# Kernel tuning notes

Measured on AMD Instinct MI355X. Metric: run time of the kernel, lower is better.

The kernel has to match this reference:

```python
import jax, jax.numpy as jnp
import numpy as np

N = 100000        # num nodes
E = 3200000       # num edges (avg degree 32)
C = 64            # num classes


def setup_inputs() -> dict:
    key = jax.random.key(0)
    k1, k2, k3 = jax.random.split(key, 3)
    edge_index = jax.random.randint(k1, (2, E), 0, N, dtype=jnp.int64)
    # Linear(N, C): weight [C, N]; we store its transpose Wt [N, C] for gather
    Wt = jax.random.normal(k2, (N, C), dtype=jnp.float32) * (1.0 / np.sqrt(N))
    b = jnp.zeros((C,), dtype=jnp.float32)
    return {"edge_index": edge_index, "Wt": Wt, "b": b}


def reference(edge_index, Wt, b):
    # logits[i] = sum_{(i,j) in edges} Wt[j] + b  == (A @ W.T + b)
    row, col = edge_index[0], edge_index[1]
    gathered = Wt[col]                                      # [E, C]
    logits = jax.ops.segment_sum(gathered, row, num_segments=N) + b  # [N, C]
    return jax.nn.log_softmax(logits, axis=1)
```

## Files before the change

kernel.cpp:

```cpp
#include <hip/hip_runtime.h>
#include <hip/hip_bf16.h>


#define C64 64
#define BROWS 64
#define LROW_SHIFT 17
#define COL_MASK 0x1FFFF
#define MAXNB 2048
#define SCAT_TPB 1024
#define SCAT_EPT2 8
#define SCAT_EDGES (SCAT_TPB * SCAT_EPT2 * 2)
#define CAPB 2432
#define GAT_TPB 512
#define FP8_SCALE 256.0f
#define FP8_ISCALE (1.0f / 256.0f)

typedef float v2f __attribute__((ext_vector_type(2)));

static __device__ __forceinline__ unsigned short f2bf(float f) {
    unsigned u = __float_as_uint(f);
    unsigned r = u + 0x7fff + ((u >> 16) & 1);
    return (unsigned short)(r >> 16);
}

__global__ __launch_bounds__(256) void LINK_cvt_bf16(const float* __restrict__ Wt,
                                                     unsigned short* __restrict__ Wtb,
                                                     int n4) {
    int i = blockIdx.x * blockDim.x + threadIdx.x;
    if (i >= n4) return;
    float4 v = ((const float4*)Wt)[i];
    ushort4 o;
    o.x = f2bf(v.x); o.y = f2bf(v.y); o.z = f2bf(v.z); o.w = f2bf(v.w);
    ((ushort4*)Wtb)[i] = o;
}

__global__ __launch_bounds__(SCAT_TPB) void LINK_cvt_scatter2(const float* __restrict__ Wt,
                                                              unsigned int* __restrict__ Wtq,
                                                              int n_u,
                                                              const int* __restrict__ ei,
                                                              int* __restrict__ cursor,
                                                              int* __restrict__ pk,
                                                              int E_, int nb, int nScat) {
    __shared__ int staged[SCAT_EDGES];
    __shared__ int h[MAXNB];
    __shared__ int lbase[MAXNB];
    __shared__ int loff[MAXNB + 1];
    __shared__ int part[SCAT_TPB];
    const int tid = threadIdx.x;

    if (blockIdx.x >= nScat) {
        int i = (blockIdx.x - nScat) * SCAT_TPB + tid;
        if (i < n_u) {
            float4 v = ((const float4*)Wt)[i];
            int p = __builtin_amdgcn_cvt_pk_fp8_f32(v.x * FP8_SCALE, v.y * FP8_SCALE, 0, false);
            p = __builtin_amdgcn_cvt_pk_fp8_f32(v.z * FP8_SCALE, v.w * FP8_SCALE, p, true);
            Wtq[i] = (unsigned)p;
        }
        return;
    }

    const int2* ei2r = (const int2*)ei;
    const int2* ei2c = (const int2*)(ei + E_);
    int2 rows[SCAT_EPT2];
    for (int i = tid; i < nb; i += SCAT_TPB) h[i] = 0;
    __syncthreads();
    const int base2 = blockIdx.x * (SCAT_TPB * SCAT_EPT2);
    const int E2 = E_ >> 1;
    #pragma unroll
    for (int i = 0; i < SCAT_EPT2; ++i) {
        int e2 = base2 + i * SCAT_TPB + tid;
        if (e2 < E2) {
            rows[i] = ei2r[e2];
            atomicAdd(&h[rows[i].x >> 6], 1);
            atomicAdd(&h[rows[i].y >> 6], 1);
        } else rows[i] = make_int2(-1, -1);
    }
    __syncthreads();

    const int chunk = (nb + SCAT_TPB - 1) / SCAT_TPB;
    const int cbeg = min(tid * chunk, nb);
    const int cend = min(cbeg + chunk, nb);
    int s = 0;
    for (int i = cbeg; i < cend; ++i) s += h[i];
    part[tid] = s;
    __syncthreads();
    for (int off = 1; off < SCAT_TPB; off <<= 1) {
        int v = (tid >= off) ? part[tid - off] : 0;
        __syncthreads();
        part[tid] += v;
        __syncthreads();
    }
    int run = (tid == 0) ? 0 : part[tid - 1];
    for (int i = cbeg; i < cend; ++i) {
        loff[i] = run;
        run += h[i];
    }
    if (tid == SCAT_TPB - 1) loff[nb] = run;
    __syncthreads();

    for (int i = tid; i < nb; i += SCAT_TPB) {
        int c = h[i];
        lbase[i] = c ? atomicAdd(&cursor[i], c) : 0;
        h[i] = 0;
    }
    __syncthreads();

    #pragma unroll
    for (int i = 0; i < SCAT_EPT2; ++i) {
        if (rows[i].x >= 0) {
            int e2 = base2 + i * SCAT_TPB + tid;
            int2 cols = ei2c[e2];
            int bkx = rows[i].x >> 6;
            int px = loff[bkx] + atomicAdd(&h[bkx], 1);
            staged[px] = ((rows[i].x & 63) << LROW_SHIFT) | cols.x;
            int bky = rows[i].y >> 6;
            int py = loff[bky] + atomicAdd(&h[bky], 1);
            staged[py] = ((rows[i].y & 63) << LROW_SHIFT) | cols.y;
        }
    }
    __syncthreads();

    const int cnt = loff[nb];
    for (int i = tid; i < cnt; i += SCAT_TPB) {
        int lo = 0, hi = nb;
        while (hi - lo > 1) {
            int mid = (lo + hi) >> 1;
            if (loff[mid] <= i) lo = mid; else hi = mid;
        }
        int gp = lbase[lo] + (i - loff[lo]);
        if (gp < CAPB) pk[lo * CAPB + gp] = staged[i];
    }
}

__global__ __launch_bounds__(SCAT_TPB) void LINK_scatter_big(const int* __restrict__ ei,
                                                             int* __restrict__ cursor,
                                                             int* __restrict__ pk,
                                                             int E_, int nb) {
    __shared__ int h[MAXNB];
    __shared__ int lbase[MAXNB];
    const int tid = threadIdx.x;
    const int2* ei2r = (const int2*)ei;
    const int2* ei2c = (const int2*)(ei + E_);
    int2 rows[SCAT_EPT2];
    for (int i = tid; i < nb; i += SCAT_TPB) h[i] = 0;
    __syncthreads();
    const int base2 = blockIdx.x * (SCAT_TPB * SCAT_EPT2);
    const int E2 = E_ >> 1;
    #pragma unroll
    for (int i = 0; i < SCAT_EPT2; ++i) {
        int e2 = base2 + i * SCAT_TPB + tid;
        if (e2 < E2) {
            rows[i] = ei2r[e2];
            atomicAdd(&h[rows[i].x >> 6], 1);
            atomicAdd(&h[rows[i].y >> 6], 1);
        } else rows[i] = make_int2(-1, -1);
    }
    __syncthreads();
    for (int i = tid; i < nb; i += SCAT_TPB) {
        int c = h[i];
        lbase[i] = c ? atomicAdd(&cursor[i], c) : 0;
    }
    __syncthreads();
    for (int i = tid; i < nb; i += SCAT_TPB) h[i] = 0;
    __syncthreads();
    #pragma unroll
    for (int i = 0; i < SCAT_EPT2; ++i) {
        if (rows[i].x >= 0) {
            int e2 = base2 + i * SCAT_TPB + tid;
            int2 cols = ei2c[e2];
            int bkx = rows[i].x >> 6;
            int lpx = lbase[bkx] + atomicAdd(&h[bkx], 1);
            if (lpx < CAPB) pk[bkx * CAPB + lpx] = ((rows[i].x & 63) << LROW_SHIFT) | cols.x;
            int bky = rows[i].y >> 6;
            int lpy = lbase[bky] + atomicAdd(&h[bky], 1);
            if (lpy < CAPB) pk[bky * CAPB + lpy] = ((rows[i].y & 63) << LROW_SHIFT) | cols.y;
        }
    }
}

__global__ __launch_bounds__(GAT_TPB) void LINK_binGather_f8(const int* __restrict__ cursor,
                                                             const int* __restrict__ pk,
                                                             const unsigned int* __restrict__ Wtq,
                                                             const float* __restrict__ b,
                                                             float* __restrict__ out,
                                                             int N_) {
    __shared__ int binned[CAPB];
    __shared__ int rcnt[BROWS];
    __shared__ int roff[BROWS];
    __shared__ int rcur[BROWS];
    const int tid = threadIdx.x;
    const int lane = tid & 63;
    const int li = lane & 15;
    const int quad = lane >> 4;
    const int w = tid >> 6;
    const int bkt = blockIdx.x;
    const int beg = bkt * CAPB;
    const int cnt = min(cursor[bkt], CAPB);

    if (tid < BROWS) rcnt[tid] = 0;
    __syncthreads();
    for (int i = tid; i < cnt; i += GAT_TPB) atomicAdd(&rcnt[pk[beg + i] >> LROW_SHIFT], 1);
    __syncthreads();
    if (tid < BROWS) {
        int v = rcnt[tid];
        int inc = v;
        #pragma unroll
        for (int d = 1; d < 64; d <<= 1) {
            int o = __shfl_up(inc, d);
            if (lane >= d) inc += o;
        }
        roff[tid] = inc - v;
        rcur[tid] = inc - v;
    }
    __syncthreads();
    for (int i = tid; i < cnt; i += GAT_TPB) {
        int p = pk[beg + i];
        int pos = atomicAdd(&rcur[p >> LROW_SHIFT], 1);
        binned[pos] = p & COL_MASK;
    }
    __syncthreads();

    const float4 bias = ((const float4*)b)[li];
    for (int r = w; r < BROWS; r += 8) {
        const int row = bkt * BROWS + r;
        if (row >= N_) break;
        const int off = roff[r];
        const int dg = rcnt[r];
        const int nq = dg >> 2;

        float a0 = 0.f, a1 = 0.f, a2 = 0.f, a3 = 0.f;
        int t = 0;
        for (; t + 8 <= nq; t += 8) {
            int cc[8];
            #pragma unroll
            for (int q = 0; q < 8; ++q) cc[q] = binned[off + 4 * (t + q) + quad];
            unsigned uu[8];
            #pragma unroll
            for (int q = 0; q < 8; ++q) uu[q] = Wtq[cc[q] * 16 + li];
            #pragma unroll
            for (int q = 0; q < 8; ++q) {
                v2f lo = __builtin_amdgcn_cvt_pk_f32_fp8((int)uu[q], false);
                v2f hi = __builtin_amdgcn_cvt_pk_f32_fp8((int)uu[q], true);
                a0 += lo[0]; a1 += lo[1]; a2 += hi[0]; a3 += hi[1];
            }
        }
        for (; t < nq; ++t) {
            int c = binned[off + 4 * t + quad];
            unsigned u = Wtq[c * 16 + li];
            v2f lo = __builtin_amdgcn_cvt_pk_f32_fp8((int)u, false);
            v2f hi = __builtin_amdgcn_cvt_pk_f32_fp8((int)u, true);
            a0 += lo[0]; a1 += lo[1]; a2 += hi[0]; a3 += hi[1];
        }
        const int rem = dg & 3;
        if (quad < rem) {
            int c = binned[off + 4 * nq + quad];
            unsigned u = Wtq[c * 16 + li];
            v2f lo = __builtin_amdgcn_cvt_pk_f32_fp8((int)u, false);
            v2f hi = __builtin_amdgcn_cvt_pk_f32_fp8((int)u, true);
            a0 += lo[0]; a1 += lo[1]; a2 += hi[0]; a3 += hi[1];
        }

        a0 += __shfl_xor(a0, 16); a0 += __shfl_xor(a0, 32);
        a1 += __shfl_xor(a1, 16); a1 += __shfl_xor(a1, 32);
        a2 += __shfl_xor(a2, 16); a2 += __shfl_xor(a2, 32);
        a3 += __shfl_xor(a3, 16); a3 += __shfl_xor(a3, 32);

        float x0 = a0 * FP8_ISCALE + bias.x;
        float x1 = a1 * FP8_ISCALE + bias.y;
        float x2 = a2 * FP8_ISCALE + bias.z;
        float x3 = a3 * FP8_ISCALE + bias.w;

        float m = fmaxf(fmaxf(x0, x1), fmaxf(x2, x3));
        #pragma unroll
        for (int mk = 1; mk < 16; mk <<= 1) m = fmaxf(m, __shfl_xor(m, mk));
        float s = __expf(x0 - m) + __expf(x1 - m) + __expf(x2 - m) + __expf(x3 - m);
        #pragma unroll
        for (int mk = 1; mk < 16; mk <<= 1) s += __shfl_xor(s, mk);
        float ls = logf(s);
        if (quad == 0) {
            float4 o;
            o.x = x0 - m - ls; o.y = x1 - m - ls; o.z = x2 - m - ls; o.w = x3 - m - ls;
            ((float4*)out)[row * 16 + li] = o;
        }
    }
}

__global__ __launch_bounds__(GAT_TPB) void LINK_binner(const int* __restrict__ cursor,
                                                       int* __restrict__ pk,
                                                       unsigned int* __restrict__ meta,
                                                       int N_) {
    __shared__ int stage[CAPB];
    __shared__ int binned[CAPB];
    __shared__ int rcnt[BROWS];
    __shared__ int roff[BROWS];
    __shared__ int rcur[BROWS];
    const int tid = threadIdx.x;
    const int lane = tid & 63;
    const int bkt = blockIdx.x;
    const int beg = bkt * CAPB;
    const int cnt = min(cursor[bkt], CAPB);

    if (tid < BROWS) rcnt[tid] = 0;
    for (int i = tid; i < cnt; i += GAT_TPB) stage[i] = pk[beg + i];
    __syncthreads();
    for (int i = tid; i < cnt; i += GAT_TPB) atomicAdd(&rcnt[stage[i] >> LROW_SHIFT], 1);
    __syncthreads();
    if (tid < BROWS) {
        int v = rcnt[tid];
        int inc = v;
        #pragma unroll
        for (int d = 1; d < 64; d <<= 1) {
            int o = __shfl_up(inc, d);
            if (lane >= d) inc += o;
        }
        roff[tid] = inc - v;
        rcur[tid] = inc - v;
    }
    __syncthreads();
    for (int i = tid; i < cnt; i += GAT_TPB) {
        int p = stage[i];
        int pos = atomicAdd(&rcur[p >> LROW_SHIFT], 1);
        binned[pos] = p & COL_MASK;
    }
    __syncthreads();
    for (int i = tid; i < cnt; i += GAT_TPB) pk[beg + i] = binned[i];
    if (tid < BROWS) {
        int row = bkt * BROWS + tid;
        if (row < N_)
            meta[row] = ((unsigned)(beg + roff[tid]) << 10) | (unsigned)min(rcnt[tid], 1023);
    }
}

__global__ __launch_bounds__(256) void LINK_gather_rows(const unsigned int* __restrict__ meta,
                                                        const int* __restrict__ scol,
                                                        const unsigned int* __restrict__ Wtu,
                                                        const float* __restrict__ b,
                                                        float* __restrict__ out,
                                                        int N_) {
    const int wid = (blockIdx.x * 256 + threadIdx.x) >> 6;
    const int nw = (gridDim.x * 256) >> 6;
    const int lane = threadIdx.x & 63;
    const int li = lane & 31;
    const int hi = lane >> 5;
    const float2 bias = ((const float2*)b)[li];

    for (int row = wid; row < N_; row += nw) {
        unsigned mt = meta[row];
        int beg = (int)(mt >> 10);
        int dg = (int)(mt & 1023);
        float l0 = 0.f, l1 = 0.f, l2 = 0.f, l3 = 0.f;
        float h0 = 0.f, h1 = 0.f, h2 = 0.f, h3 = 0.f;
        int npair = dg >> 1;
        int t = 0;
        for (; t + 8 <= npair; t += 8) {
            int cc[8];
            #pragma unroll
            for (int q = 0; q < 8; ++q) cc[q] = scol[beg + 2 * (t + q) + hi];
            unsigned uu[8];
            #pragma unroll
            for (int q = 0; q < 8; ++q) uu[q] = Wtu[cc[q] * 32 + li];
            l0 += __uint_as_float(uu[0] << 16); h0 += __uint_as_float(uu[0] & 0xffff0000u);
            l1 += __uint_as_float(uu[1] << 16); h1 += __uint_as_float(uu[1] & 0xffff0000u);
            l2 += __uint_as_float(uu[2] << 16); h2 += __uint_as_float(uu[2] & 0xffff0000u);
            l3 += __uint_as_float(uu[3] << 16); h3 += __uint_as_float(uu[3] & 0xffff0000u);
            l0 += __uint_as_float(uu[4] << 16); h0 += __uint_as_float(uu[4] & 0xffff0000u);
            l1 += __uint_as_float(uu[5] << 16); h1 += __uint_as_float(uu[5] & 0xffff0000u);
            l2 += __uint_as_float(uu[6] << 16); h2 += __uint_as_float(uu[6] & 0xffff0000u);
            l3 += __uint_as_float(uu[7] << 16); h3 += __uint_as_float(uu[7] & 0xffff0000u);
        }
        for (; t < npair; ++t) {
            int c = scol[beg + 2 * t + hi];
            unsigned u = Wtu[c * 32 + li];
            l0 += __uint_as_float(u << 16);
            h0 += __uint_as_float(u & 0xffff0000u);
        }
        if (dg & 1) {
            int c = scol[beg + dg - 1];
            if (hi == 0) {
                unsigned u = Wtu[c * 32 + li];
                l0 += __uint_as_float(u << 16);
                h0 += __uint_as_float(u & 0xffff0000u);
            }
        }
        float x0 = (l0 + l1) + (l2 + l3);
        float x1 = (h0 + h1) + (h2 + h3);
        x0 += __shfl_xor(x0, 32);
        x1 += __shfl_xor(x1, 32);
        x0 += bias.x;
        x1 += bias.y;
        float m = fmaxf(x0, x1);
        #pragma unroll
        for (int mk = 1; mk < 32; mk <<= 1) m = fmaxf(m, __shfl_xor(m, mk));
        float s = __expf(x0 - m) + __expf(x1 - m);
        #pragma unroll
        for (int mk = 1; mk < 32; mk <<= 1) s += __shfl_xor(s, mk);
        float ls = logf(s);
        if (hi == 0) {
            float2 o; o.x = x0 - m - ls; o.y = x1 - m - ls;
            ((float2*)out)[row * 32 + li] = o;
        }
    }
}

__global__ void LINK_scatter_atomic(const int* __restrict__ ei, const float* __restrict__ Wt,
                                    float* __restrict__ logits, int E_) {
    int t = blockIdx.x * blockDim.x + threadIdx.x;
    int e = t >> 6;
    int c = t & 63;
    if (e >= E_) return;
    atomicAdd(&logits[ei[e] * C64 + c], Wt[ei[E_ + e] * C64 + c]);
}
__global__ void LINK_lsm_inplace(float* __restrict__ logits, const float* __restrict__ b, int N_) {
    int wave = (blockIdx.x * blockDim.x + threadIdx.x) >> 6;
    int c = threadIdx.x & 63;
    if (wave >= N_) return;
    float x = logits[wave * C64 + c] + b[c];
    float m = x;
    #pragma unroll
    for (int mk = 1; mk < 64; mk <<= 1) m = fmaxf(m, __shfl_xor(m, mk));
    float s = __expf(x - m);
    #pragma unroll
    for (int mk = 1; mk < 64; mk <<= 1) s += __shfl_xor(s, mk);
    logits[wave * C64 + c] = x - m - logf(s);
}

extern "C" void kernel_launch(void* const* d_in, const int* in_sizes, int n_in,
                              void* d_out, int out_size, void* d_ws, size_t ws_size,
                              hipStream_t stream) {
    const int*   ei = (const int*)d_in[0];
    const float* Wt = (const float*)d_in[1];
    const float* b  = (const float*)d_in[2];
    float* out = (float*)d_out;

    const int E_ = in_sizes[0] / 2;
    const int C_ = in_sizes[2];
    const int N_ = in_sizes[1] / C_;
    const int nb = (N_ + BROWS - 1) / BROWS;

    const int n4 = N_ * C_ / 4;
    char* ws = (char*)d_ws;
    const bool c_ok = (C_ == 64) && ((N_ * C_) % 4 == 0) && (E_ % 2 == 0);

    size_t a_cursor = 0;
    size_t a_pk     = ((size_t)nb * 4 + 255) & ~(size_t)255;
    size_t a_wtq    = (a_pk + (size_t)nb * CAPB * 4 + 255) & ~(size_t)255;
    size_t a_need   = a_wtq + (size_t)N_ * C_;

    size_t b_cursor = 0;
    size_t b_pk     = ((size_t)nb * 4 + 255) & ~(size_t)255;
    size_t b_wtb    = (b_pk + (size_t)nb * CAPB * 4 + 255) & ~(size_t)255;
    size_t b_meta   = (b_wtb + (size_t)N_ * C_ * 2 + 255) & ~(size_t)255;
    size_t b_need   = b_meta + (size_t)N_ * 4;

    const int nScat = (E_ + SCAT_EDGES - 1) / SCAT_EDGES;

    if (c_ok && nb <= MAXNB && ws_size >= a_need) {
        int* cursor = (int*)(ws + a_cursor);
        int* pk     = (int*)(ws + a_pk);
        unsigned int* Wtq = (unsigned int*)(ws + a_wtq);

        hipMemsetAsync(cursor, 0, (size_t)nb * 4, stream);
        const int nCvt = (n4 + SCAT_TPB - 1) / SCAT_TPB;
        LINK_cvt_scatter2<<<nScat + nCvt, SCAT_TPB, 0, stream>>>(
            Wt, Wtq, n4, ei, cursor, pk, E_, nb, nScat);
        LINK_binGather_f8<<<nb, GAT_TPB, 0, stream>>>(cursor, pk, Wtq, b, out, N_);
        return;
    }
    if (c_ok && nb <= MAXNB && ws_size >= b_need) {
        int* cursor = (int*)(ws + b_cursor);
        int* pk     = (int*)(ws + b_pk);
        unsigned short* Wtb = (unsigned short*)(ws + b_wtb);
        unsigned int* meta = (unsigned int*)(ws + b_meta);

        LINK_cvt_bf16<<<(n4 + 255) / 256, 256, 0, stream>>>(Wt, Wtb, n4);
        hipMemsetAsync(cursor, 0, (size_t)nb * 4, stream);
        LINK_scatter_big<<<nScat, SCAT_TPB, 0, stream>>>(ei, cursor, pk, E_, nb);
        LINK_binner<<<nb, GAT_TPB, 0, stream>>>(cursor, pk, meta, N_);
        LINK_gather_rows<<<4096, 256, 0, stream>>>(meta, pk, (const unsigned int*)Wtb, b, out, N_);
        return;
    }

    hipMemsetAsync(d_out, 0, (size_t)N_ * C_ * sizeof(float), stream);
    long long threads = (long long)E_ * 64;
    LINK_scatter_atomic<<<(int)((threads + 255) / 256), 256, 0, stream>>>(ei, Wt, out, E_);
    LINK_lsm_inplace<<<(N_ * 64 + 255) / 256, 256, 0, stream>>>(out, b, N_);
}
```

Before: 99.91 us.

## Gather fp8 rows with 16-byte loads, four rows per wavefront, staged output

The gather kernel is restructured so each wavefront handles four rows at once. Each lane loads a full 16-byte uint4 of fp8 weights instead of a 4-byte word, and accumulates 16 channels in registers. Output rows are staged in shared memory and written as coalesced float4 stores. The aim is fewer, wider memory transactions per edge and more memory parallelism. In exchange it uses more registers, and lanes idle when the four rows have uneven degrees, since every row runs to the group's maximum degree.

```diff
diff --git a/kernel.cpp b/kernel.cpp
--- a/kernel.cpp
+++ b/kernel.cpp
@@ -22,6 +22,23 @@
     unsigned r = u + 0x7fff + ((u >> 16) & 1);
     return (unsigned short)(r >> 16);
 }
+
+#define DECODE16(U, ACC)                                                        \
+    do {                                                                        \
+        v2f lo_, hi_;                                                           \
+        lo_ = __builtin_amdgcn_cvt_pk_f32_fp8((int)(U).x, false);               \
+        hi_ = __builtin_amdgcn_cvt_pk_f32_fp8((int)(U).x, true);                \
+        ACC[0] += lo_[0]; ACC[1] += lo_[1]; ACC[2] += hi_[0]; ACC[3] += hi_[1]; \
+        lo_ = __builtin_amdgcn_cvt_pk_f32_fp8((int)(U).y, false);               \
+        hi_ = __builtin_amdgcn_cvt_pk_f32_fp8((int)(U).y, true);                \
+        ACC[4] += lo_[0]; ACC[5] += lo_[1]; ACC[6] += hi_[0]; ACC[7] += hi_[1]; \
+        lo_ = __builtin_amdgcn_cvt_pk_f32_fp8((int)(U).z, false);               \
+        hi_ = __builtin_amdgcn_cvt_pk_f32_fp8((int)(U).z, true);                \
+        ACC[8] += lo_[0]; ACC[9] += lo_[1]; ACC[10] += hi_[0]; ACC[11] += hi_[1];\
+        lo_ = __builtin_amdgcn_cvt_pk_f32_fp8((int)(U).w, false);               \
+        hi_ = __builtin_amdgcn_cvt_pk_f32_fp8((int)(U).w, true);                \
+        ACC[12] += lo_[0]; ACC[13] += lo_[1]; ACC[14] += hi_[0]; ACC[15] += hi_[1];\
+    } while (0)
 
 __global__ __launch_bounds__(256) void LINK_cvt_bf16(const float* __restrict__ Wt,
                                                      unsigned short* __restrict__ Wtb,
@@ -178,21 +195,23 @@
     }
 }
 
-__global__ __launch_bounds__(GAT_TPB) void LINK_binGather_f8(const int* __restrict__ cursor,
-                                                             const int* __restrict__ pk,
-                                                             const unsigned int* __restrict__ Wtq,
-                                                             const float* __restrict__ b,
-                                                             float* __restrict__ out,
-                                                             int N_) {
+__global__ __launch_bounds__(GAT_TPB) void LINK_binGather_f8w(const int* __restrict__ cursor,
+                                                              const int* __restrict__ pk,
+                                                              const unsigned int* __restrict__ Wtq,
+                                                              const float* __restrict__ b,
+                                                              float* __restrict__ out,
+                                                              int N_) {
     __shared__ int binned[CAPB];
     __shared__ int rcnt[BROWS];
     __shared__ int roff[BROWS];
     __shared__ int rcur[BROWS];
+    __shared__ float smout[8][256];
     const int tid = threadIdx.x;
     const int lane = tid & 63;
-    const int li = lane & 15;
-    const int quad = lane >> 4;
     const int w = tid >> 6;
+    const int rq = (lane >> 4) & 3;
+    const int slot = (lane >> 2) & 3;
+    const int qt = lane & 3;
     const int bkt = blockIdx.x;
     const int beg = bkt * CAPB;
     const int cnt = min(cursor[bkt], CAPB);
@@ -220,67 +239,91 @@
     }
     __syncthreads();
 
-    const float4 bias = ((const float4*)b)[li];
-    for (int r = w; r < BROWS; r += 8) {
-        const int row = bkt * BROWS + r;
-        if (row >= N_) break;
+    const uint4* W4 = (const uint4*)Wtq;
+
+    for (int qq = 0; qq < 2; ++qq) {
+        const int qidx = (w << 1) + qq;
+        const int r = qidx * 4 + rq;
         const int off = roff[r];
         const int dg = rcnt[r];
-        const int nq = dg >> 2;
-
-        float a0 = 0.f, a1 = 0.f, a2 = 0.f, a3 = 0.f;
+        int dgm = dg;
+        dgm = max(dgm, __shfl_xor(dgm, 16));
+        dgm = max(dgm, __shfl_xor(dgm, 32));
+        const int steps = (dgm + 3) >> 2;
+
+        float acc[16];
+        #pragma unroll
+        for (int k = 0; k < 16; ++k) acc[k] = 0.f;
+
         int t = 0;
-        for (; t + 8 <= nq; t += 8) {
-            int cc[8];
+        for (; t + 4 <= steps; t += 4) {
+            uint4 u[4];
             #pragma unroll
-            for (int q = 0; q < 8; ++q) cc[q] = binned[off + 4 * (t + q) + quad];
-            unsigned uu[8];
+            for (int j = 0; j < 4; ++j) {
+                int eidx = (t + j) * 4 + slot;
+                uint4 uu = make_uint4(0u, 0u, 0u, 0u);
+                if (eidx < dg) {
+                    int c = binned[off + eidx];
+                    uu = W4[c * 4 + qt];
+                }
+                u[j] = uu;
+            }
             #pragma unroll
-            for (int q = 0; q < 8; ++q) uu[q] = Wtq[cc[q] * 16 + li];
+            for (int j = 0; j < 4; ++j) DECODE16(u[j], acc);
+        }
+        for (; t < steps; ++t) {
+            int eidx = t * 4 + slot;
+            if (eidx < dg) {
+                int c = binned[off + eidx];
+                uint4 uu = W4[c * 4 + qt];
+                DECODE16(uu, acc);
+            }
+        }
+
+        #pragma unroll
+        for (int k = 0; k < 16; ++k) {
+            acc[k] += __shfl_xor(acc[k], 4);
+            acc[k] += __shfl_xor(acc[k], 8);
+        }
+
+        #pragma unroll
+        for (int k = 0; k < 4; ++k) {
+            float4 bb = ((const float4*)b)[qt * 4 + k];
+            acc[4 * k + 0] = acc[4 * k + 0] * FP8_ISCALE + bb.x;
+            acc[4 * k + 1] = acc[4 * k + 1] * FP8_ISCALE + bb.y;
+            acc[4 * k + 2] = acc[4 * k + 2] * FP8_ISCALE + bb.z;
+            acc[4 * k + 3] = acc[4 * k + 3] * FP8_ISCALE + bb.w;
+        }
+        float m = acc[0];
+        #pragma unroll
+        for (int k = 1; k < 16; ++k) m = fmaxf(m, acc[k]);
+        m = fmaxf(m, __shfl_xor(m, 1));
+        m = fmaxf(m, __shfl_xor(m, 2));
+        float s = 0.f;
+        #pragma unroll
+        for (int k = 0; k < 16; ++k) s += __expf(acc[k] - m);
+        s += __shfl_xor(s, 1);
+        s += __shfl_xor(s, 2);
+        const float ls = logf(s) + m;
+
+        if (slot == 0) {
             #pragma unroll
-            for (int q = 0; q < 8; ++q) {
-                v2f lo = __builtin_amdgcn_cvt_pk_f32_fp8((int)uu[q], false);
-                v2f hi = __builtin_amdgcn_cvt_pk_f32_fp8((int)uu[q], true);
-                a0 += lo[0]; a1 += lo[1]; a2 += hi[0]; a3 += hi[1];
+            for (int k = 0; k < 4; ++k) {
+                float4 o;
+                o.x = acc[4 * k + 0] - ls;
+                o.y = acc[4 * k + 1] - ls;
+                o.z = acc[4 * k + 2] - ls;
+                o.w = acc[4 * k + 3] - ls;
+                ((float4*)&smout[w][0])[rq * 16 + qt * 4 + k] = o;
             }
         }
-        for (; t < nq; ++t) {
-            int c = binned[off + 4 * t + quad];
-            unsigned u = Wtq[c * 16 + li];
-            v2f lo = __builtin_amdgcn_cvt_pk_f32_fp8((int)u, false);
-            v2f hi = __builtin_amdgcn_cvt_pk_f32_fp8((int)u, true);
-            a0 += lo[0]; a1 += lo[1]; a2 += hi[0]; a3 += hi[1];
-        }
-        const int rem = dg & 3;
-        if (quad < rem) {
-            int c = binned[off + 4 * nq + quad];
-            unsigned u = Wtq[c * 16 + li];
-            v2f lo = __builtin_amdgcn_cvt_pk_f32_fp8((int)u, false);
-            v2f hi = __builtin_amdgcn_cvt_pk_f32_fp8((int)u, true);
-            a0 += lo[0]; a1 += lo[1]; a2 += hi[0]; a3 += hi[1];
-        }
-
-        a0 += __shfl_xor(a0, 16); a0 += __shfl_xor(a0, 32);
-        a1 += __shfl_xor(a1, 16); a1 += __shfl_xor(a1, 32);
-        a2 += __shfl_xor(a2, 16); a2 += __shfl_xor(a2, 32);
-        a3 += __shfl_xor(a3, 16); a3 += __shfl_xor(a3, 32);
-
-        float x0 = a0 * FP8_ISCALE + bias.x;
-        float x1 = a1 * FP8_ISCALE + bias.y;
-        float x2 = a2 * FP8_ISCALE + bias.z;
-        float x3 = a3 * FP8_ISCALE + bias.w;
-
-        float m = fmaxf(fmaxf(x0, x1), fmaxf(x2, x3));
-        #pragma unroll
-        for (int mk = 1; mk < 16; mk <<= 1) m = fmaxf(m, __shfl_xor(m, mk));
-        float s = __expf(x0 - m) + __expf(x1 - m) + __expf(x2 - m) + __expf(x3 - m);
-        #pragma unroll
-        for (int mk = 1; mk < 16; mk <<= 1) s += __shfl_xor(s, mk);
-        float ls = logf(s);
-        if (quad == 0) {
-            float4 o;
-            o.x = x0 - m - ls; o.y = x1 - m - ls; o.z = x2 - m - ls; o.w = x3 - m - ls;
-            ((float4*)out)[row * 16 + li] = o;
+        {
+            const int qlo = qidx * 4;
+            const int row = bkt * BROWS + qlo + (lane >> 4);
+            if (row < N_) {
+                float4 o = ((const float4*)&smout[w][0])[lane];
+                ((float4*)out)[(bkt * BROWS + qlo) * 16 + lane] = o;
+            }
         }
     }
 }
@@ -463,7 +506,7 @@
         const int nCvt = (n4 + SCAT_TPB - 1) / SCAT_TPB;
         LINK_cvt_scatter2<<<nScat + nCvt, SCAT_TPB, 0, stream>>>(
             Wt, Wtq, n4, ei, cursor, pk, E_, nb, nScat);
-        LINK_binGather_f8<<<nb, GAT_TPB, 0, stream>>>(cursor, pk, Wtq, b, out, N_);
+        LINK_binGather_f8w<<<nb, GAT_TPB, 0, stream>>>(cursor, pk, Wtq, b, out, N_);
         return;
     }
     if (c_ok && nb <= MAXNB && ws_size >= b_need) {
```

After: 93.72 us. 1.07x faster.
